# Performance work log

Measured on AMD Instinct MI355X. Metric: run time of the kernel, lower is better.

The kernel has to match this reference:

```python
import jax, jax.numpy as jnp
import numpy as np

N = 100000      # nodes
E = 1600000     # edges
HID = 128       # hidden_dim
HEADS = 4
C = HID // HEADS  # 32 per-head channels
L = 2           # num_layers
G = 64          # graphs in batch


def setup_inputs() -> dict:
    key = jax.random.key(0)
    ks = jax.random.split(key, 24)
    s = 0.1
    inp = {
        'x': jax.random.normal(ks[0], (N, 1), jnp.float32),
        'edge_attr': jax.random.normal(ks[1], (E, 1), jnp.float32),
        'edge_index': jax.random.randint(ks[2], (2, E), 0, N, jnp.int32),
        'batch': jnp.sort(jax.random.randint(ks[3], (N,), 0, G, jnp.int32)),
        # encoders
        'enc_w': jax.random.normal(ks[4], (1, HID), jnp.float32) * s,
        'enc_b': jax.random.normal(ks[5], (HID,), jnp.float32) * s,
        'eenc_w': jax.random.normal(ks[6], (1, HID), jnp.float32) * s,
        'eenc_b': jax.random.normal(ks[7], (HID,), jnp.float32) * s,
        # GATConv params, stacked over layers
        'lin_w': jax.random.normal(ks[8], (L, HID, HID), jnp.float32) * s,
        'att_src': jax.random.normal(ks[9], (L, HEADS, C), jnp.float32) * s,
        'att_dst': jax.random.normal(ks[10], (L, HEADS, C), jnp.float32) * s,
        'att_edge': jax.random.normal(ks[11], (L, HEADS, C), jnp.float32) * s,
        'lin_edge_w': jax.random.normal(ks[12], (L, HID, HID), jnp.float32) * s,
        'conv_b': jax.random.normal(ks[13], (L, HID), jnp.float32) * s,
        # BatchNorm (eval mode, running stats)
        'bn_gamma': jax.random.uniform(ks[14], (L, HID), jnp.float32, 0.5, 1.5),
        'bn_beta': jax.random.normal(ks[15], (L, HID), jnp.float32) * s,
        'bn_mean': jax.random.normal(ks[16], (L, HID), jnp.float32) * s,
        'bn_var': jax.random.uniform(ks[17], (L, HID), jnp.float32, 0.5, 1.5),
        # classifier (num_classes==2 path -> sigmoid, squeeze)
        'w1': jax.random.normal(ks[18], (HID, HID // 2), jnp.float32) * s,
        'b1': jax.random.normal(ks[19], (HID // 2,), jnp.float32) * s,
        'w2': jax.random.normal(ks[20], (HID // 2, 1), jnp.float32) * s,
        'b2': jax.random.normal(ks[21], (1,), jnp.float32) * s,
    }
    return inp


def reference(x, edge_attr, edge_index, batch, enc_w, enc_b, eenc_w, eenc_b,
              lin_w, att_src, att_dst, att_edge, lin_edge_w, conv_b,
              bn_gamma, bn_beta, bn_mean, bn_var, w1, b1, w2, b2):
    src, dst = edge_index[0], edge_index[1]
    h = x @ enc_w + enc_b                      # [N, HID]
    e = edge_attr @ eenc_w + eenc_b            # [E, HID]
    n = h.shape[0]
    nL, H, Ch = att_src.shape[0], att_src.shape[1], att_src.shape[2]
    for l in range(nL):
        identity = h
        xs = (h @ lin_w[l]).reshape(n, H, Ch)            # [N, H, C]
        ee = (e @ lin_edge_w[l]).reshape(-1, H, Ch)      # [E, H, C]
        a_s = jnp.einsum('nhc,hc->nh', xs, att_src[l])
        a_d = jnp.einsum('nhc,hc->nh', xs, att_dst[l])
        a_e = jnp.einsum('ehc,hc->eh', ee, att_edge[l])
        alpha = jax.nn.leaky_relu(a_s[src] + a_d[dst] + a_e, 0.2)  # [E, H]
        # segment softmax over edges grouped by destination node
        amax = jax.ops.segment_max(alpha, dst, num_segments=n)
        amax = jax.lax.stop_gradient(jnp.where(jnp.isfinite(amax), amax, 0.0))
        p = jnp.exp(alpha - amax[dst])
        denom = jax.ops.segment_sum(p, dst, num_segments=n)
        attn = p / (denom[dst] + 1e-16)                  # [E, H]
        msg = (xs[src] * attn[:, :, None]).reshape(-1, H * Ch)
        out = jax.ops.segment_sum(msg, dst, num_segments=n) + conv_b[l]
        # BatchNorm1d (eval mode)
        out = (out - bn_mean[l]) * jax.lax.rsqrt(bn_var[l] + 1e-5) * bn_gamma[l] + bn_beta[l]
        h = jax.nn.relu(out) + identity
    # global mean pool
    cnt = jax.ops.segment_sum(jnp.ones((n,), h.dtype), batch, num_segments=G)
    pooled = jax.ops.segment_sum(h, batch, num_segments=G) / jnp.maximum(cnt, 1.0)[:, None]
    z = jax.nn.relu(pooled @ w1 + b1)
    return jax.nn.sigmoid(z @ w2 + b2)[:, 0]   # [G]
```

## Files before the change

### kernel.cpp

```cpp
#include <hip/hip_runtime.h>
#include <hip/hip_bf16.h>

#define NN 100000
#define EE 1600000
#define HIDD 128
#define GG 64
#define NB 512
#define NPB 196
#define NCH 391
#define CH 4096

typedef short bf16x8 __attribute__((ext_vector_type(8)));
typedef float f32x4 __attribute__((ext_vector_type(4)));

__device__ inline unsigned int f2bf(float f) {
    unsigned int u = __float_as_uint(f);
    return (u + 0x7FFFu + ((u >> 16) & 1u)) >> 16;
}
__device__ inline unsigned int pk2(float a, float b) { return f2bf(a) | (f2bf(b) << 16); }
__device__ inline float blo(unsigned int u) { return __uint_as_float(u << 16); }
__device__ inline float bhi(unsigned int u) { return __uint_as_float(u & 0xFFFF0000u); }


__global__ __launch_bounds__(256) void k_bhist(const int* __restrict__ ei,
                                               int* __restrict__ wg_hist) {
    __shared__ int cnt[NB];
    int t = threadIdx.x;
    cnt[t] = 0; cnt[t + 256] = 0;
    __syncthreads();
    int e0 = blockIdx.x * CH;
    #pragma unroll
    for (int i = 0; i < CH / 256; ++i) {
        int e = e0 + i * 256 + t;
        if (e < EE) {
            unsigned d = (unsigned)ei[EE + e];
            atomicAdd(&cnt[d / NPB], 1);
        }
    }
    __syncthreads();
    wg_hist[blockIdx.x * NB + t] = cnt[t];
    wg_hist[blockIdx.x * NB + 256 + t] = cnt[t + 256];
}

__global__ __launch_bounds__(512) void k_bscan_col(const int* __restrict__ wg_hist,
                                                   int* __restrict__ ofs,
                                                   int* __restrict__ btot) {
    __shared__ int sd[512];
    int b = blockIdx.x;
    int t = threadIdx.x;
    int v = (t < NCH) ? wg_hist[t * NB + b] : 0;
    sd[t] = v;
    __syncthreads();
    for (int off = 1; off < 512; off <<= 1) {
        int u = (t >= off) ? sd[t - off] : 0;
        __syncthreads();
        sd[t] += u;
        __syncthreads();
    }
    if (t < NCH) ofs[t * NB + b] = sd[t] - v;
    if (t == 511) btot[b] = sd[511];
}

__global__ __launch_bounds__(512) void k_bbase(const int* __restrict__ btot,
                                               int* __restrict__ bbase) {
    __shared__ int sd[512];
    int t = threadIdx.x;
    int v = btot[t];
    sd[t] = v;
    __syncthreads();
    for (int off = 1; off < 512; off <<= 1) {
        int u = (t >= off) ? sd[t - off] : 0;
        __syncthreads();
        sd[t] += u;
        __syncthreads();
    }
    bbase[t] = sd[t] - v;
    if (t == 511) bbase[512] = sd[511];
}

__global__ __launch_bounds__(256) void k_bscatter(const int* __restrict__ ei,
                                                  const float* __restrict__ ea,
                                                  const int* __restrict__ ofs,
                                                  const int* __restrict__ bbase,
                                                  uint2* __restrict__ ebuf) {
    __shared__ int lcnt[NB];
    __shared__ int sofs[NB];
    int t = threadIdx.x;
    lcnt[t] = 0; lcnt[t + 256] = 0;
    sofs[t] = ofs[blockIdx.x * NB + t] + bbase[t];
    sofs[t + 256] = ofs[blockIdx.x * NB + 256 + t] + bbase[t + 256];
    __syncthreads();
    int e0 = blockIdx.x * CH;
    #pragma unroll
    for (int i = 0; i < CH / 256; ++i) {
        int e = e0 + i * 256 + t;
        if (e < EE) {
            unsigned s = (unsigned)ei[e];
            unsigned d = (unsigned)ei[EE + e];
            float w = ea[e];
            unsigned b = d / NPB;
            unsigned dloc = d - b * NPB;
            int r = atomicAdd(&lcnt[b], 1);
            ebuf[sofs[b] + r] = make_uint2(s | (dloc << 17), __float_as_uint(w));
        }
    }
}

__global__ __launch_bounds__(256) void k_bsort(const uint2* __restrict__ ebuf,
                                               const int* __restrict__ bbase,
                                               uint2* __restrict__ csr,
                                               int* __restrict__ row_ptr) {
    __shared__ int cnt[NPB];
    __shared__ int sc[256];
    __shared__ int pos[NPB];
    int b = blockIdx.x;
    int t = threadIdx.x;
    int ebeg = bbase[b], eend = bbase[b + 1];
    int n0 = b * NPB;
    int nn = NN - n0; if (nn > NPB) nn = NPB;
    if (t < NPB) cnt[t] = 0;
    __syncthreads();
    for (int j = ebeg + t; j < eend; j += 256) {
        uint2 r = ebuf[j];
        atomicAdd(&cnt[r.x >> 17], 1);
    }
    __syncthreads();
    int v = (t < NPB) ? cnt[t] : 0;
    sc[t] = v;
    __syncthreads();
    for (int off = 1; off < 256; off <<= 1) {
        int u = (t >= off) ? sc[t - off] : 0;
        __syncthreads();
        sc[t] += u;
        __syncthreads();
    }
    int lofs = sc[t] - v;
    if (t < NPB) {
        pos[t] = lofs;
        if (t < nn) row_ptr[n0 + t] = ebeg + lofs;
    }
    __syncthreads();
    for (int j = ebeg + t; j < eend; j += 256) {
        uint2 r = ebuf[j];
        int dloc = r.x >> 17;
        int slot = ebeg + atomicAdd(&pos[dloc], 1);
        csr[slot] = make_uint2(r.x & 0x1FFFFu, r.y);
    }
    if (b == 0 && t == 0) row_ptr[NN] = EE;
}


__global__ void k_derive(const float* __restrict__ enc_w, const float* __restrict__ enc_b,
                         const float* __restrict__ eenc_w, const float* __restrict__ eenc_b,
                         const float* __restrict__ lin_w, const float* __restrict__ lin_edge_w,
                         const float* __restrict__ att_src, const float* __restrict__ att_dst,
                         const float* __restrict__ att_edge,
                         const float* __restrict__ bn_gamma, const float* __restrict__ bn_beta,
                         const float* __restrict__ bn_mean, const float* __restrict__ bn_var,
                         float* __restrict__ cblk, unsigned short* __restrict__ wpk16) {
    int t = threadIdx.x;
    __shared__ float red[128];

    float P = 0.f, Q = 0.f;
    for (int j = 0; j < 128; ++j) {
        float w = lin_w[j * 128 + t];
        P += enc_w[j] * w;
        Q += enc_b[j] * w;
    }
    cblk[t] = P;
    cblk[128 + t] = Q;

    for (int l = 0; l < 2; ++l) {
        float sc = bn_gamma[l * 128 + t] * rsqrtf(bn_var[l * 128 + t] + 1e-5f);
        cblk[256 + l * 128 + t] = sc;
        cblk[512 + l * 128 + t] = bn_beta[l * 128 + t] - bn_mean[l * 128 + t] * sc;
    }

    for (int k = 0; k < 128; ++k) {
        wpk16[t * 128 + k] = (unsigned short)f2bf(lin_w[16384 + k * 128 + t]);
    }

    auto headred = [&](float v, int outbase) {
        red[t] = v;
        __syncthreads();
        if (t < 4) {
            float s = 0.f;
            for (int c = 0; c < 32; ++c) s += red[t * 32 + c];
            cblk[outbase + t] = s;
        }
        __syncthreads();
    };

    headred(P * att_src[t], 768);
    headred(Q * att_src[t], 772);
    headred(P * att_dst[t], 776);
    headred(Q * att_dst[t], 780);

    for (int l = 0; l < 2; ++l) {
        float W1 = 0.f, W2 = 0.f;
        for (int j = 0; j < 128; ++j) {
            float w = lin_edge_w[l * 16384 + j * 128 + t];
            W1 += eenc_w[j] * w;
            W2 += eenc_b[j] * w;
        }
        headred(W1 * att_edge[l * 128 + t], 784 + l * 4);
        headred(W2 * att_edge[l * 128 + t], 792 + l * 4);
    }
}


__global__ __launch_bounds__(256) void k_l0(const uint2* __restrict__ csr,
                                            const int* __restrict__ row_ptr,
                                            const float* __restrict__ x,
                                            const float* __restrict__ cblk,
                                            float* __restrict__ tmp0) {
    int wid = threadIdx.x >> 6, lane = threadIdx.x & 63;
    int n = blockIdx.x * 4 + wid;
    if (n >= NN) return;
    int h = lane & 3, eo = lane >> 2;
    float xdv = x[n];
    float ps = cblk[768 + h], qs = cblk[772 + h];
    float base = xdv * cblk[776 + h] + cblk[780 + h] + cblk[792 + h];
    float au = cblk[784 + h];
    int jb = row_ptr[n], je = row_ptr[n + 1];
    float s = 0.f, sx = 0.f;
    for (int j0 = jb; j0 < je; j0 += 16) {
        int j = j0 + eo;
        if (j < je) {
            uint2 r = csr[j];
            float xsv = x[r.x];
            float w = __uint_as_float(r.y);
            float a = xsv * ps + qs + base + w * au;
            a = (a > 0.f) ? a : 0.2f * a;
            float p = __expf(a);
            s += p;
            sx += p * xsv;
        }
    }
    #pragma unroll
    for (int off = 4; off < 64; off <<= 1) {
        s += __shfl_xor(s, off, 64);
        sx += __shfl_xor(sx, off, 64);
    }
    if (lane < 4) {
        tmp0[(size_t)n * 8 + lane] = s;
        tmp0[(size_t)n * 8 + 4 + lane] = sx;
    }
}

__global__ void k_l0_epi(const float* __restrict__ x, const float* __restrict__ enc_w,
                         const float* __restrict__ enc_b, const float* __restrict__ conv_b,
                         const float* __restrict__ cblk, const float* __restrict__ tmp0,
                         float* __restrict__ hbuf, unsigned short* __restrict__ h16) {
    int idx = blockIdx.x * blockDim.x + threadIdx.x;
    if (idx >= NN * HIDD) return;
    int n = idx >> 7, k = idx & 127, h = (k >> 5) & 3;
    float s = tmp0[n * 8 + h];
    float sx = tmp0[n * 8 + 4 + h];
    float inv = 1.f / (s + 1e-16f);
    float agg = (sx * cblk[k] + s * cblk[128 + k]) * inv + conv_b[k];
    float o = agg * cblk[256 + k] + cblk[512 + k];
    float hv = fmaxf(o, 0.f) + x[n] * enc_w[k] + enc_b[k];
    hbuf[idx] = hv;
    h16[idx] = (unsigned short)f2bf(hv);
}


__global__ __launch_bounds__(256) void k_gemm_mfma(const unsigned short* __restrict__ h16,
                                                   const unsigned short* __restrict__ wpk,
                                                   unsigned short* __restrict__ xs16) {
    int wid = threadIdx.x >> 6, lane = threadIdx.x & 63;
    int rbase = blockIdx.x * 64 + wid * 16;
    int hi = lane >> 4, c15 = lane & 15;

    const bf16x8* hrow = (const bf16x8*)(h16 + (size_t)(rbase + c15) * 128);
    bf16x8 a0 = hrow[hi];
    bf16x8 a1 = hrow[4 + hi];
    bf16x8 a2 = hrow[8 + hi];
    bf16x8 a3 = hrow[12 + hi];

    f32x4 acc[8];
    #pragma unroll
    for (int t8 = 0; t8 < 8; ++t8) {
        const bf16x8* wrow = (const bf16x8*)(wpk + (size_t)(t8 * 16 + c15) * 128);
        f32x4 a_ = {0.f, 0.f, 0.f, 0.f};
        a_ = __builtin_amdgcn_mfma_f32_16x16x32_bf16(a0, wrow[hi], a_, 0, 0, 0);
        a_ = __builtin_amdgcn_mfma_f32_16x16x32_bf16(a1, wrow[4 + hi], a_, 0, 0, 0);
        a_ = __builtin_amdgcn_mfma_f32_16x16x32_bf16(a2, wrow[8 + hi], a_, 0, 0, 0);
        a_ = __builtin_amdgcn_mfma_f32_16x16x32_bf16(a3, wrow[12 + hi], a_, 0, 0, 0);
        acc[t8] = a_;
    }
    #pragma unroll
    for (int j = 0; j < 4; ++j) {
        size_t rb = (size_t)(rbase + hi * 4 + j) * 128;
        #pragma unroll
        for (int t8 = 0; t8 < 8; ++t8) {
            xs16[rb + t8 * 16 + c15] = (unsigned short)f2bf(acc[t8][j]);
        }
    }
}

__global__ void k_asad(const unsigned short* __restrict__ xs16,
                       const float* __restrict__ att_src1, const float* __restrict__ att_dst1,
                       float* __restrict__ a_s, float* __restrict__ a_d) {
    int wid = threadIdx.x >> 6, lane = threadIdx.x & 63;
    int n = blockIdx.x * 4 + wid;
    if (n >= NN) return;
    unsigned int u = *(const unsigned int*)(xs16 + (size_t)n * 128 + lane * 2);
    float v0 = blo(u), v1 = bhi(u);
    float2 as2 = *(const float2*)(att_src1 + lane * 2);
    float2 ad2 = *(const float2*)(att_dst1 + lane * 2);
    float vs = v0 * as2.x + v1 * as2.y;
    float vd = v0 * ad2.x + v1 * ad2.y;
    #pragma unroll
    for (int off = 1; off < 16; off <<= 1) {
        vs += __shfl_xor(vs, off, 64);
        vd += __shfl_xor(vd, off, 64);
    }
    if ((lane & 15) == 0) {
        a_s[n * 4 + (lane >> 4)] = vs;
        a_d[n * 4 + (lane >> 4)] = vd;
    }
}


__global__ __launch_bounds__(256) void k_l1_agg(const unsigned short* __restrict__ xs16,
                                                const uint2* __restrict__ csr,
                                                const float* __restrict__ a_s,
                                                const float* __restrict__ a_d,
                                                const int* __restrict__ row_ptr,
                                                const float* __restrict__ cblk,
                                                const float* __restrict__ conv_b,
                                                float* __restrict__ hbuf) {
    int wid = threadIdx.x >> 6, lane = threadIdx.x & 63;
    int n = blockIdx.x * 4 + wid;
    if (n >= NN) return;
    int h = lane >> 4;
    int c0 = lane * 2;

    float adh = a_d[(size_t)n * 4 + h] + cblk[796 + h];
    float au = cblk[788 + h];

    float acc0 = 0.f, acc1 = 0.f, s = 0.f;
    int jb = row_ptr[n], je = row_ptr[n + 1];
    const char* xb = (const char*)xs16;
    int j = jb;
    for (; j + 7 < je; j += 8) {
        uint2 r[8];
        float as[8];
        unsigned int u[8];
        #pragma unroll
        for (int q = 0; q < 8; ++q) r[q] = csr[j + q];
        #pragma unroll
        for (int q = 0; q < 8; ++q) as[q] = a_s[(size_t)r[q].x * 4 + h];
        #pragma unroll
        for (int q = 0; q < 8; ++q)
            u[q] = *(const unsigned int*)(xb + ((size_t)r[q].x << 8) + (lane << 2));
        #pragma unroll
        for (int q = 0; q < 8; ++q) {
            float al = as[q] + adh + __uint_as_float(r[q].y) * au;
            al = (al > 0.f) ? al : 0.2f * al;
            float p = __expf(al);
            s += p;
            acc0 += p * blo(u[q]);
            acc1 += p * bhi(u[q]);
        }
    }
    for (; j + 3 < je; j += 4) {
        uint2 r[4];
        float as[4];
        unsigned int u[4];
        #pragma unroll
        for (int q = 0; q < 4; ++q) r[q] = csr[j + q];
        #pragma unroll
        for (int q = 0; q < 4; ++q) as[q] = a_s[(size_t)r[q].x * 4 + h];
        #pragma unroll
        for (int q = 0; q < 4; ++q)
            u[q] = *(const unsigned int*)(xb + ((size_t)r[q].x << 8) + (lane << 2));
        #pragma unroll
        for (int q = 0; q < 4; ++q) {
            float al = as[q] + adh + __uint_as_float(r[q].y) * au;
            al = (al > 0.f) ? al : 0.2f * al;
            float p = __expf(al);
            s += p;
            acc0 += p * blo(u[q]);
            acc1 += p * bhi(u[q]);
        }
    }
    for (; j < je; ++j) {
        uint2 r0 = csr[j];
        float as0 = a_s[(size_t)r0.x * 4 + h];
        unsigned int u0 = *(const unsigned int*)(xb + ((size_t)r0.x << 8) + (lane << 2));
        float al0 = as0 + adh + __uint_as_float(r0.y) * au;
        al0 = (al0 > 0.f) ? al0 : 0.2f * al0;
        float p0 = __expf(al0);
        s += p0;
        acc0 += p0 * blo(u0);
        acc1 += p0 * bhi(u0);
    }
    float inv = 1.f / (s + 1e-16f);
    float o0 = acc0 * inv + conv_b[128 + c0];
    float o1 = acc1 * inv + conv_b[128 + c0 + 1];
    o0 = o0 * cblk[384 + c0] + cblk[640 + c0];
    o1 = o1 * cblk[384 + c0 + 1] + cblk[640 + c0 + 1];
    float2* hp = (float2*)(hbuf + (size_t)n * 128 + c0);
    float2 hv = *hp;
    hv.x += fmaxf(o0, 0.f);
    hv.y += fmaxf(o1, 0.f);
    *hp = hv;
}


__global__ void k_pool(const float* __restrict__ hbuf, const int* __restrict__ batch,
                       float* __restrict__ pooled, float* __restrict__ gcnt) {
    int t = threadIdx.x;
    int n0 = blockIdx.x * 256;
    int nend = min(n0 + 256, NN);
    float acc = 0.f;
    int run = 0;
    int gprev = batch[n0];
    for (int n = n0; n < nend; ++n) {
        int g = batch[n];
        if (g != gprev) {
            atomicAdd(&pooled[gprev * 128 + t], acc);
            if (t == 0) atomicAdd(&gcnt[gprev], (float)run);
            acc = 0.f;
            run = 0;
            gprev = g;
        }
        acc += hbuf[(size_t)n * 128 + t];
        run++;
    }
    atomicAdd(&pooled[gprev * 128 + t], acc);
    if (t == 0) atomicAdd(&gcnt[gprev], (float)run);
}

__global__ void k_head(const float* __restrict__ pooled, const float* __restrict__ gcnt,
                       const float* __restrict__ w1, const float* __restrict__ b1,
                       const float* __restrict__ w2, const float* __restrict__ b2,
                       float* __restrict__ out) {
    int g = blockIdx.x;
    int j = threadIdx.x;
    float inv = 1.f / fmaxf(gcnt[g], 1.f);
    float acc = b1[j];
    for (int k = 0; k < 128; ++k) acc += pooled[g * 128 + k] * inv * w1[k * 64 + j];
    float z = fmaxf(acc, 0.f);
    float v = z * w2[j];
    #pragma unroll
    for (int off = 32; off; off >>= 1) v += __shfl_down(v, off, 64);
    if (j == 0) out[g] = 1.f / (1.f + __expf(-(v + b2[0])));
}


extern "C" void kernel_launch(void* const* d_in, const int* in_sizes, int n_in,
                              void* d_out, int out_size, void* d_ws, size_t ws_size,
                              hipStream_t stream) {
    const float* x        = (const float*)d_in[0];
    const float* ea       = (const float*)d_in[1];
    const int*   ei       = (const int*)d_in[2];
    const int*   batch    = (const int*)d_in[3];
    const float* enc_w    = (const float*)d_in[4];
    const float* enc_b    = (const float*)d_in[5];
    const float* eenc_w   = (const float*)d_in[6];
    const float* eenc_b   = (const float*)d_in[7];
    const float* lin_w    = (const float*)d_in[8];
    const float* att_src  = (const float*)d_in[9];
    const float* att_dst  = (const float*)d_in[10];
    const float* att_edge = (const float*)d_in[11];
    const float* lin_edge = (const float*)d_in[12];
    const float* conv_b   = (const float*)d_in[13];
    const float* bn_gamma = (const float*)d_in[14];
    const float* bn_beta  = (const float*)d_in[15];
    const float* bn_mean  = (const float*)d_in[16];
    const float* bn_var   = (const float*)d_in[17];
    const float* w1       = (const float*)d_in[18];
    const float* b1       = (const float*)d_in[19];
    const float* w2       = (const float*)d_in[20];
    const float* b2       = (const float*)d_in[21];
    float* out = (float*)d_out;

    char* ws = (char*)d_ws;
    size_t off = 0;
    auto alloc = [&](size_t bytes) {
        size_t o = off;
        off = (off + bytes + 511) & ~(size_t)511;
        return o;
    };
    int*    wg_hist = (int*)(ws + alloc((size_t)NCH * NB * 4));
    int*    ofs     = (int*)(ws + alloc((size_t)NCH * NB * 4));
    int*    btot    = (int*)(ws + alloc(NB * 4));
    int*    bbase   = (int*)(ws + alloc((NB + 1) * 4));
    int*    row_ptr = (int*)(ws + alloc((size_t)(NN + 1) * 4));
    uint2*  ebuf    = (uint2*)(ws + alloc((size_t)EE * 8));
    uint2*  csr     = (uint2*)(ws + alloc((size_t)EE * 8));
    float*  cblk    = (float*)(ws + alloc(1024 * 4));
    unsigned short* wpk16 = (unsigned short*)(ws + alloc(128 * 128 * 2));
    float*  tmp0    = (float*)(ws + alloc((size_t)NN * 8 * 4));
    float*  a_s     = (float*)(ws + alloc((size_t)NN * 4 * 4));
    float*  a_d     = (float*)(ws + alloc((size_t)NN * 4 * 4));
    float*  hbuf    = (float*)(ws + alloc((size_t)NN * HIDD * 4));
    unsigned short* h16  = (unsigned short*)(ws + alloc((size_t)(NN + 64) * HIDD * 2));
    unsigned short* xs16 = (unsigned short*)(ws + alloc((size_t)(NN + 64) * HIDD * 2));
    float*  pooled  = (float*)(ws + alloc(GG * HIDD * 4 + GG * 4));
    float*  gcnt    = pooled + GG * HIDD;

    hipMemsetAsync(pooled, 0, GG * HIDD * 4 + GG * 4, stream);

    const int nparts = (NN + 255) / 256;
    const int nwave4 = (NN + 3) / 4;

    k_bhist<<<NCH, 256, 0, stream>>>(ei, wg_hist);
    k_bscan_col<<<NB, 512, 0, stream>>>(wg_hist, ofs, btot);
    k_bbase<<<1, 512, 0, stream>>>(btot, bbase);
    k_bscatter<<<NCH, 256, 0, stream>>>(ei, ea, ofs, bbase, ebuf);
    k_bsort<<<511, 256, 0, stream>>>(ebuf, bbase, csr, row_ptr);

    k_derive<<<1, 128, 0, stream>>>(enc_w, enc_b, eenc_w, eenc_b, lin_w, lin_edge,
                                    att_src, att_dst, att_edge,
                                    bn_gamma, bn_beta, bn_mean, bn_var, cblk, wpk16);

    k_l0<<<nwave4, 256, 0, stream>>>(csr, row_ptr, x, cblk, tmp0);
    k_l0_epi<<<(NN * HIDD + 255) / 256, 256, 0, stream>>>(x, enc_w, enc_b, conv_b, cblk,
                                                          tmp0, hbuf, h16);

    k_gemm_mfma<<<(NN + 63) / 64, 256, 0, stream>>>(h16, wpk16, xs16);
    k_asad<<<nwave4, 256, 0, stream>>>(xs16, att_src + 128, att_dst + 128, a_s, a_d);
    k_l1_agg<<<nwave4, 256, 0, stream>>>(xs16, csr, a_s, a_d, row_ptr, cblk, conv_b, hbuf);

    k_pool<<<nparts, 128, 0, stream>>>(hbuf, batch, pooled, gcnt);
    k_head<<<GG, 64, 0, stream>>>(pooled, gcnt, w1, b1, w2, b2, out);
}
```

Before: 439.6 us.

## Cooperative edge loading in layer-1 aggregation and bf16 residual output to pool

The layer-1 aggregation kernel now has the 16 lanes of each head load 16 CSR entries at once, compute their attention weights in parallel, and broadcast weight and source index by shuffle before gathering features. This replaces the redundant per-lane loads of csr and a_s and the serial exp work. The kernel also writes the activated output as bf16 to a separate buffer instead of doing a read-modify-write on the fp32 hbuf, and the pool kernel adds the two. This cuts global traffic, at the cost of bf16 rounding on the layer-1 output and an extra shuffle loop with variable trip count.

```diff
diff --git a/kernel.cpp b/kernel.cpp
--- a/kernel.cpp
+++ b/kernel.cpp
@@ -331,87 +331,54 @@
                                                 const int* __restrict__ row_ptr,
                                                 const float* __restrict__ cblk,
                                                 const float* __restrict__ conv_b,
-                                                float* __restrict__ hbuf) {
+                                                unsigned short* __restrict__ outb) {
     int wid = threadIdx.x >> 6, lane = threadIdx.x & 63;
     int n = blockIdx.x * 4 + wid;
     if (n >= NN) return;
-    int h = lane >> 4;
+    int hh = lane >> 4;
+    int q = lane & 15;
     int c0 = lane * 2;
-
-    float adh = a_d[(size_t)n * 4 + h] + cblk[796 + h];
-    float au = cblk[788 + h];
-
-    float acc0 = 0.f, acc1 = 0.f, s = 0.f;
+    int base = lane & 48;
+
+    float adh = a_d[(size_t)n * 4 + hh] + cblk[796 + hh];
+    float au = cblk[788 + hh];
+
+    float acc0 = 0.f, acc1 = 0.f, spart = 0.f;
     int jb = row_ptr[n], je = row_ptr[n + 1];
     const char* xb = (const char*)xs16;
-    int j = jb;
-    for (; j + 7 < je; j += 8) {
-        uint2 r[8];
-        float as[8];
-        unsigned int u[8];
-        #pragma unroll
-        for (int q = 0; q < 8; ++q) r[q] = csr[j + q];
-        #pragma unroll
-        for (int q = 0; q < 8; ++q) as[q] = a_s[(size_t)r[q].x * 4 + h];
-        #pragma unroll
-        for (int q = 0; q < 8; ++q)
-            u[q] = *(const unsigned int*)(xb + ((size_t)r[q].x << 8) + (lane << 2));
-        #pragma unroll
-        for (int q = 0; q < 8; ++q) {
-            float al = as[q] + adh + __uint_as_float(r[q].y) * au;
-            al = (al > 0.f) ? al : 0.2f * al;
-            float p = __expf(al);
-            s += p;
-            acc0 += p * blo(u[q]);
-            acc1 += p * bhi(u[q]);
-        }
-    }
-    for (; j + 3 < je; j += 4) {
-        uint2 r[4];
-        float as[4];
-        unsigned int u[4];
-        #pragma unroll
-        for (int q = 0; q < 4; ++q) r[q] = csr[j + q];
-        #pragma unroll
-        for (int q = 0; q < 4; ++q) as[q] = a_s[(size_t)r[q].x * 4 + h];
-        #pragma unroll
-        for (int q = 0; q < 4; ++q)
-            u[q] = *(const unsigned int*)(xb + ((size_t)r[q].x << 8) + (lane << 2));
-        #pragma unroll
-        for (int q = 0; q < 4; ++q) {
-            float al = as[q] + adh + __uint_as_float(r[q].y) * au;
-            al = (al > 0.f) ? al : 0.2f * al;
-            float p = __expf(al);
-            s += p;
-            acc0 += p * blo(u[q]);
-            acc1 += p * bhi(u[q]);
-        }
-    }
-    for (; j < je; ++j) {
-        uint2 r0 = csr[j];
-        float as0 = a_s[(size_t)r0.x * 4 + h];
-        unsigned int u0 = *(const unsigned int*)(xb + ((size_t)r0.x << 8) + (lane << 2));
-        float al0 = as0 + adh + __uint_as_float(r0.y) * au;
-        al0 = (al0 > 0.f) ? al0 : 0.2f * al0;
-        float p0 = __expf(al0);
-        s += p0;
-        acc0 += p0 * blo(u0);
-        acc1 += p0 * bhi(u0);
-    }
+    for (int j0 = jb; j0 < je; j0 += 16) {
+        int ne = je - j0; if (ne > 16) ne = 16;
+        uint2 r = (q < ne) ? csr[j0 + q] : make_uint2(0u, 0u);
+        float as = a_s[(size_t)r.x * 4 + hh];
+        float al = as + adh + __uint_as_float(r.y) * au;
+        al = (al > 0.f) ? al : 0.2f * al;
+        float p = (q < ne) ? __expf(al) : 0.f;
+        spart += p;
+        for (int q2 = 0; q2 < ne; ++q2) {
+            float pq = __shfl(p, base | q2, 64);
+            int srcq = __shfl((int)r.x, base | q2, 64);
+            unsigned int u = *(const unsigned int*)(xb + ((size_t)srcq << 8) + (lane << 2));
+            acc0 += pq * blo(u);
+            acc1 += pq * bhi(u);
+        }
+    }
+    float s = spart;
+    s += __shfl_xor(s, 1, 64);
+    s += __shfl_xor(s, 2, 64);
+    s += __shfl_xor(s, 4, 64);
+    s += __shfl_xor(s, 8, 64);
     float inv = 1.f / (s + 1e-16f);
     float o0 = acc0 * inv + conv_b[128 + c0];
     float o1 = acc1 * inv + conv_b[128 + c0 + 1];
     o0 = o0 * cblk[384 + c0] + cblk[640 + c0];
     o1 = o1 * cblk[384 + c0 + 1] + cblk[640 + c0 + 1];
-    float2* hp = (float2*)(hbuf + (size_t)n * 128 + c0);
-    float2 hv = *hp;
-    hv.x += fmaxf(o0, 0.f);
-    hv.y += fmaxf(o1, 0.f);
-    *hp = hv;
-}
-
-
-__global__ void k_pool(const float* __restrict__ hbuf, const int* __restrict__ batch,
+    unsigned int pk = pk2(fmaxf(o0, 0.f), fmaxf(o1, 0.f));
+    *(unsigned int*)(outb + (size_t)n * 128 + c0) = pk;
+}
+
+
+__global__ void k_pool(const float* __restrict__ hbuf, const unsigned short* __restrict__ outb,
+                       const int* __restrict__ batch,
                        float* __restrict__ pooled, float* __restrict__ gcnt) {
     int t = threadIdx.x;
     int n0 = blockIdx.x * 256;
@@ -428,7 +395,9 @@
             run = 0;
             gprev = g;
         }
-        acc += hbuf[(size_t)n * 128 + t];
+        float hv = hbuf[(size_t)n * 128 + t];
+        unsigned short ub = outb[(size_t)n * 128 + t];
+        acc += hv + __uint_as_float(((unsigned int)ub) << 16);
         run++;
     }
     atomicAdd(&pooled[gprev * 128 + t], acc);
@@ -501,6 +470,7 @@
     float*  hbuf    = (float*)(ws + alloc((size_t)NN * HIDD * 4));
     unsigned short* h16  = (unsigned short*)(ws + alloc((size_t)(NN + 64) * HIDD * 2));
     unsigned short* xs16 = (unsigned short*)(ws + alloc((size_t)(NN + 64) * HIDD * 2));
+    unsigned short* outb = (unsigned short*)(ws + alloc((size_t)NN * HIDD * 2));
     float*  pooled  = (float*)(ws + alloc(GG * HIDD * 4 + GG * 4));
     float*  gcnt    = pooled + GG * HIDD;
 
@@ -525,8 +495,8 @@
 
     k_gemm_mfma<<<(NN + 63) / 64, 256, 0, stream>>>(h16, wpk16, xs16);
     k_asad<<<nwave4, 256, 0, stream>>>(xs16, att_src + 128, att_dst + 128, a_s, a_d);
-    k_l1_agg<<<nwave4, 256, 0, stream>>>(xs16, csr, a_s, a_d, row_ptr, cblk, conv_b, hbuf);
-
-    k_pool<<<nparts, 128, 0, stream>>>(hbuf, batch, pooled, gcnt);
+    k_l1_agg<<<nwave4, 256, 0, stream>>>(xs16, csr, a_s, a_d, row_ptr, cblk, conv_b, outb);
+
+    k_pool<<<nparts, 128, 0, stream>>>(hbuf, outb, batch, pooled, gcnt);
     k_head<<<GG, 64, 0, stream>>>(pooled, gcnt, w1, b1, w2, b2, out);
 }
```

Result: slower. 499.0 us (+13.5%).
